# Performance work log

Measured on AMD Instinct MI355X. Metric: run time of the kernel, lower is better.

## Reference

```python
import jax, jax.numpy as jnp
import numpy as np

B, S, D, H = 2048, 200, 64, 4
H1, H2 = 64, 32
F = 4 * D


def _prelu(x, a):
    return jnp.where(x > 0, x, a * x)


def setup_inputs() -> dict:
    key = jax.random.key(0)
    ks = jax.random.split(key, 12)
    inp = {
        "query": jax.random.normal(ks[0], (B, D), dtype=jnp.float32),
        "keys": jax.random.normal(ks[1], (B, S, D), dtype=jnp.float32),
        "keys_mask": jax.random.randint(ks[2], (B, S), 0, 2, dtype=jnp.int32),
        # per-head MLP params (torch Linear equivalent, stored as [in,out])
        "W1": jax.random.normal(ks[3], (H, F, H1), dtype=jnp.float32) / np.sqrt(F),
        "b1": jnp.zeros((H, H1), dtype=jnp.float32),
        "a1": jnp.full((H,), 0.25, dtype=jnp.float32),  # PReLU weight
        "W2": jax.random.normal(ks[4], (H, H1, H2), dtype=jnp.float32) / np.sqrt(H1),
        "b2": jnp.zeros((H, H2), dtype=jnp.float32),
        "a2": jnp.full((H,), 0.25, dtype=jnp.float32),
        "W3": jax.random.normal(ks[5], (H, H2), dtype=jnp.float32) / np.sqrt(H2),
        "b3": jnp.zeros((H,), dtype=jnp.float32),
        # output projection
        "Wo": jax.random.normal(ks[6], (D, D), dtype=jnp.float32) / np.sqrt(D),
        "bo": jnp.zeros((D,), dtype=jnp.float32),
    }
    return inp


def reference(query, keys, keys_mask, W1, b1, a1, W2, b2, a2, W3, b3, Wo, bo):
    # rich attention features: [keys, q, keys*q, keys-q] -> [B,S,4D]
    q = jnp.broadcast_to(query[:, None, :], keys.shape)
    x = jnp.concatenate([keys, q, keys * q, keys - q], axis=-1)
    # all heads at once: tiny per-head MLP with PReLU
    h = jnp.einsum('bsf,hfk->bhsk', x, W1) + b1[None, :, None, :]   # [B,H,S,H1]
    h = _prelu(h, a1[None, :, None, None])
    h = jnp.einsum('bhsk,hkm->bhsm', h, W2) + b2[None, :, None, :]  # [B,H,S,H2]
    h = _prelu(h, a2[None, :, None, None])
    scores = jnp.einsum('bhsm,hm->bhs', h, W3) + b3[None, :, None]  # [B,H,S]
    # mask + softmax + NaN->0 (all-masked rows)
    valid = (keys_mask != 0)[:, None, :]
    scores = jnp.where(valid, scores, -jnp.inf)
    w = jax.nn.softmax(scores, axis=-1)
    w = jnp.where(jnp.isnan(w), jnp.zeros_like(w), w)
    # weighted sum over keys, mean over heads
    out_h = jnp.einsum('bhs,bsd->bhd', w, keys)  # [B,H,D]
    combined = out_h.mean(axis=1)                # [B,D]
    return combined @ Wo + bo
```

## Files before the change

kernel.cpp:

```cpp
#include <hip/hip_runtime.h>
#include <math.h>

constexpr int B  = 2048;
constexpr int S  = 200;
constexpr int D  = 64;
constexpr int H  = 4;
constexpr int H1 = 64;
constexpr int H2 = 32;
constexpr int F  = 256;

constexpr int PK = 72;

typedef short bf16x8 __attribute__((ext_vector_type(8)));
typedef float f32x4  __attribute__((ext_vector_type(4)));
typedef unsigned uint4v __attribute__((ext_vector_type(4)));

__device__ __forceinline__ unsigned cvtpk(float a, float b) {
    unsigned r;
    asm volatile("v_cvt_pk_bf16_f32 %0, %1, %2" : "=v"(r) : "v"(a), "v"(b));
    return r;
}
__device__ __forceinline__ float lo16f(unsigned w) { return __builtin_bit_cast(float, w << 16); }
__device__ __forceinline__ float hi16f(unsigned w) { return __builtin_bit_cast(float, w & 0xffff0000u); }

constexpr size_t SAD_OFF = 0;
constexpr size_t SC_OFF  = SAD_OFF + 4 * 4096 * 4;
constexpr size_t SBD_OFF = SC_OFF  + 4 * 4096 * 4;
constexpr size_t W2I_OFF = SBD_OFF + 4 * 4096 * 4;

__global__ __launch_bounds__(256) void build_kernel(
    const float* __restrict__ W1, const float* __restrict__ W2,
    float* __restrict__ sad, float* __restrict__ sc, float* __restrict__ sbd,
    ushort* __restrict__ w2i)
{
    const int h = blockIdx.x;
    const int t = threadIdx.x;
    const float* w1h = W1 + (size_t)h * F * H1;

    #pragma unroll
    for (int half = 0; half < 2; ++half) {
        const int sl = half * 256 + t;
        const int f  = sl >> 6, l = sl & 63;
        const int mt = f & 3, kk = f >> 2;
        const int k  = 16 * mt + (l & 15);
        const int d0 = 32 * kk + ((l >> 4) << 3);
        float vs[8], vc[8], vb[8];
        #pragma unroll
        for (int j = 0; j < 8; ++j) {
            const int d = d0 + j;
            float A  = w1h[d * 64 + k];
            float Bv = w1h[(64 + d) * 64 + k];
            float C  = w1h[(128 + d) * 64 + k];
            float Dv = w1h[(192 + d) * 64 + k];
            vs[j] = A + Dv; vc[j] = C; vb[j] = Bv - Dv;
        }
        const size_t off = ((size_t)h * 512 + sl) * 8;
        *(f32x4*)&sad[off]     = *(f32x4*)&vs[0];
        *(f32x4*)&sad[off + 4] = *(f32x4*)&vs[4];
        *(f32x4*)&sc [off]     = *(f32x4*)&vc[0];
        *(f32x4*)&sc [off + 4] = *(f32x4*)&vc[4];
        *(f32x4*)&sbd[off]     = *(f32x4*)&vb[0];
        *(f32x4*)&sbd[off + 4] = *(f32x4*)&vb[4];
    }

    {
        const int f2 = t >> 6, l = t & 63;
        const int mt2 = f2 & 1, w = f2 >> 1;
        const int m = 16 * mt2 + (l & 15), k20 = 32 * w + ((l >> 4) << 3);
        const float* w2h = W2 + (size_t)h * H1 * H2;
        uint4v u = { cvtpk(w2h[(k20 + 0) * 32 + m], w2h[(k20 + 1) * 32 + m]),
                     cvtpk(w2h[(k20 + 2) * 32 + m], w2h[(k20 + 3) * 32 + m]),
                     cvtpk(w2h[(k20 + 4) * 32 + m], w2h[(k20 + 5) * 32 + m]),
                     cvtpk(w2h[(k20 + 6) * 32 + m], w2h[(k20 + 7) * 32 + m]) };
        *(uint4v*)&w2i[((size_t)h * 4 + f2) * 512 + l * 8] = u;
    }
}

__global__ __launch_bounds__(256, 3) void fused_b_kernel(
    const float* __restrict__ query, const float* __restrict__ keys,
    const int* __restrict__ mask,
    const float* __restrict__ sad, const float* __restrict__ sc,
    const float* __restrict__ sbd, const ushort* __restrict__ w2i,
    const float* __restrict__ b1, const float* __restrict__ a1,
    const float* __restrict__ b2, const float* __restrict__ a2,
    const float* __restrict__ W3, const float* __restrict__ b3,
    const float* __restrict__ Wo, const float* __restrict__ bo,
    float* __restrict__ out)
{
    __shared__ ushort sK[200 * PK];
    __shared__ ushort relay[4][16 * PK];

    const int b    = blockIdx.x;
    const int t    = threadIdx.x;
    const int lane = t & 63;
    const int h    = t >> 6;
    const int g    = lane >> 4;
    const int ln16 = lane & 15;

    unsigned mbits = 0;
    {
        int mval[4];
        #pragma unroll
        for (int c = 0; c < 4; ++c) {
            int s = lane + 64 * c;
            mval[c] = (s < S) ? mask[(size_t)b * S + s] : 0;
        }
        #pragma unroll
        for (int st = 0; st < 13; ++st) {
            const int src = 16 * (st & 3) + ln16;
            int v = (st >> 2) == 0 ? __shfl(mval[0], src)
                  : (st >> 2) == 1 ? __shfl(mval[1], src)
                  : (st >> 2) == 2 ? __shfl(mval[2], src)
                  :                  __shfl(mval[3], src);
            mbits |= (v != 0) ? (1u << st) : 0u;
        }
    }

    {
        const float4* k4 = (const float4*)(keys + (size_t)b * S * D);
        for (int idx = t; idx < S * D / 4; idx += 256) {
            float4 v = k4[idx];
            int s = idx >> 4, dc = (idx & 15) * 4;
            *(uint2*)&sK[s * PK + dc] = make_uint2(cvtpk(v.x, v.y), cvtpk(v.z, v.w));
        }
    }

    const float* qb = query + (size_t)b * D;
    bf16x8 wh[4][2];
    float qtp0 = 0.f, qtp1 = 0.f, qtp2 = 0.f, qtp3 = 0.f;
    #pragma unroll
    for (int kk = 0; kk < 2; ++kk) {
        const int d0 = 32 * kk + 8 * g;
        f32x4 q0 = *(const f32x4*)&qb[d0];
        f32x4 q1 = *(const f32x4*)&qb[d0 + 4];
        #pragma unroll
        for (int mt = 0; mt < 4; ++mt) {
            const int f = kk * 4 + mt;
            const size_t off = ((size_t)h * 512 + f * 64 + lane) * 8;
            f32x4 s0 = *(const f32x4*)&sad[off], s1 = *(const f32x4*)&sad[off + 4];
            f32x4 c0 = *(const f32x4*)&sc [off], c1 = *(const f32x4*)&sc [off + 4];
            f32x4 bd0 = *(const f32x4*)&sbd[off], bd1 = *(const f32x4*)&sbd[off + 4];
            float w0 = s0[0] + q0[0] * c0[0], w1 = s0[1] + q0[1] * c0[1];
            float w2 = s0[2] + q0[2] * c0[2], w3 = s0[3] + q0[3] * c0[3];
            float w4 = s1[0] + q1[0] * c1[0], w5 = s1[1] + q1[1] * c1[1];
            float w6 = s1[2] + q1[2] * c1[2], w7 = s1[3] + q1[3] * c1[3];
            uint4v u = { cvtpk(w0, w1), cvtpk(w2, w3), cvtpk(w4, w5), cvtpk(w6, w7) };
            wh[mt][kk] = __builtin_bit_cast(bf16x8, u);
            float d = q0[0]*bd0[0] + q0[1]*bd0[1] + q0[2]*bd0[2] + q0[3]*bd0[3]
                    + q1[0]*bd1[0] + q1[1]*bd1[1] + q1[2]*bd1[2] + q1[3]*bd1[3];
            if (mt == 0) qtp0 += d; else if (mt == 1) qtp1 += d;
            else if (mt == 2) qtp2 += d; else qtp3 += d;
        }
    }
    qtp0 += __shfl_xor(qtp0, 16); qtp0 += __shfl_xor(qtp0, 32);
    qtp1 += __shfl_xor(qtp1, 16); qtp1 += __shfl_xor(qtp1, 32);
    qtp2 += __shfl_xor(qtp2, 16); qtp2 += __shfl_xor(qtp2, 32);
    qtp3 += __shfl_xor(qtp3, 16); qtp3 += __shfl_xor(qtp3, 32);
    f32x4 qtv[4];
    #pragma unroll
    for (int mt = 0; mt < 4; ++mt) {
        float src = (mt == 0) ? qtp0 : (mt == 1) ? qtp1 : (mt == 2) ? qtp2 : qtp3;
        f32x4 b1v = *(const f32x4*)&b1[h * 64 + mt * 16 + 4 * g];
        f32x4 v;
        #pragma unroll
        for (int i = 0; i < 4; ++i) v[i] = __shfl(src, 4 * g + i) + b1v[i];
        qtv[mt] = v;
    }

    bf16x8 w2f[2][2];
    #pragma unroll
    for (int w = 0; w < 2; ++w)
        #pragma unroll
        for (int mt2 = 0; mt2 < 2; ++mt2)
            w2f[w][mt2] = *(const bf16x8*)&w2i[((size_t)h * 4 + w * 2 + mt2) * 512 + lane * 8];
    f32x4 b2v[2], w3v[2];
    #pragma unroll
    for (int mt2 = 0; mt2 < 2; ++mt2) {
        b2v[mt2] = *(const f32x4*)&b2[h * 32 + mt2 * 16 + 4 * g];
        w3v[mt2] = *(const f32x4*)&W3[h * 32 + mt2 * 16 + 4 * g];
    }
    const float a1v = a1[h], a2v = a2[h], b3v = b3[h];

    __syncthreads();

    ushort* myR = relay[h];
    float sc13[13];

    #pragma unroll
    for (int st = 0; st < 13; ++st) {
        int srow = st * 16 + ln16;
        srow = srow > 199 ? 199 : srow;
        bf16x8 bk0 = *(const bf16x8*)&sK[srow * PK + 0  + 8 * g];
        bf16x8 bk1 = *(const bf16x8*)&sK[srow * PK + 32 + 8 * g];

        f32x4 acc[4] = { qtv[0], qtv[1], qtv[2], qtv[3] };
        #pragma unroll
        for (int mt = 0; mt < 4; ++mt)
            acc[mt] = __builtin_amdgcn_mfma_f32_16x16x32_bf16(wh[mt][0], bk0, acc[mt], 0, 0, 0);
        #pragma unroll
        for (int mt = 0; mt < 4; ++mt)
            acc[mt] = __builtin_amdgcn_mfma_f32_16x16x32_bf16(wh[mt][1], bk1, acc[mt], 0, 0, 0);

        #pragma unroll
        for (int mt = 0; mt < 4; ++mt) {
            float v0 = acc[mt][0]; v0 = v0 > 0.f ? v0 : a1v * v0;
            float v1 = acc[mt][1]; v1 = v1 > 0.f ? v1 : a1v * v1;
            float v2 = acc[mt][2]; v2 = v2 > 0.f ? v2 : a1v * v2;
            float v3 = acc[mt][3]; v3 = v3 > 0.f ? v3 : a1v * v3;
            *(uint2*)&myR[ln16 * PK + mt * 16 + 4 * g] =
                make_uint2(cvtpk(v0, v1), cvtpk(v2, v3));
        }

        f32x4 acc2[2] = { b2v[0], b2v[1] };
        #pragma unroll
        for (int w = 0; w < 2; ++w) {
            bf16x8 Bh = *(const bf16x8*)&myR[ln16 * PK + w * 32 + 8 * g];
            #pragma unroll
            for (int mt2 = 0; mt2 < 2; ++mt2)
                acc2[mt2] = __builtin_amdgcn_mfma_f32_16x16x32_bf16(w2f[w][mt2], Bh, acc2[mt2], 0, 0, 0);
        }

        float part = 0.f;
        #pragma unroll
        for (int mt2 = 0; mt2 < 2; ++mt2) {
            #pragma unroll
            for (int i = 0; i < 4; ++i) {
                float v = acc2[mt2][i];
                v = v > 0.f ? v : a2v * v;
                part += v * w3v[mt2][i];
            }
        }
        part += __shfl_xor(part, 16);
        part += __shfl_xor(part, 32);
        sc13[st] = part + b3v;
    }

    float* ws = (float*)myR;
    {
        float M = -INFINITY;
        #pragma unroll
        for (int st = 0; st < 13; ++st)
            if ((mbits >> st) & 1) M = fmaxf(M, sc13[st]);
        #pragma unroll
        for (int off = 1; off < 16; off <<= 1) M = fmaxf(M, __shfl_xor(M, off));
        float Z = 0.f;
        #pragma unroll
        for (int st = 0; st < 13; ++st)
            Z += ((mbits >> st) & 1) ? __expf(sc13[st] - M) : 0.f;
        #pragma unroll
        for (int off = 1; off < 16; off <<= 1) Z += __shfl_xor(Z, off);
        const float inv = Z > 0.f ? 1.f / Z : 0.f;
        if (g == 0) {
            #pragma unroll
            for (int st = 0; st < 13; ++st) {
                const int s = st * 16 + ln16;
                if (st < 12 || ln16 < 8)
                    ws[s] = ((mbits >> st) & 1) ? __expf(sc13[st] - M) * inv : 0.f;
            }
        }
    }

    {
        const int sg = lane >> 4, dq = ln16;
        float ax = 0.f, ay = 0.f, az = 0.f, aw = 0.f;
        #pragma unroll 5
        for (int i = 0; i < 50; ++i) {
            const int s = sg * 50 + i;
            const float w = ws[s];
            uint2 kv = *(const uint2*)&sK[s * PK + 4 * dq];
            ax += w * lo16f(kv.x); ay += w * hi16f(kv.x);
            az += w * lo16f(kv.y); aw += w * hi16f(kv.y);
        }
        ax += __shfl_xor(ax, 16); ay += __shfl_xor(ay, 16);
        az += __shfl_xor(az, 16); aw += __shfl_xor(aw, 16);
        ax += __shfl_xor(ax, 32); ay += __shfl_xor(ay, 32);
        az += __shfl_xor(az, 32); aw += __shfl_xor(aw, 32);
        if (lane < 16) {
            float4 o = { ax, ay, az, aw };
            *(float4*)&ws[200 + 4 * dq] = o;
        }
    }
    __syncthreads();

    {
        float p = 0.f;
        #pragma unroll
        for (int j = 0; j < 16; ++j) {
            const int d = 16 * h + j;
            const float cmb = 0.25f * (((const float*)relay[0])[200 + d]
                                     + ((const float*)relay[1])[200 + d]
                                     + ((const float*)relay[2])[200 + d]
                                     + ((const float*)relay[3])[200 + d]);
            p += cmb * Wo[d * 64 + lane];
        }
        ws[264 + lane] = p;
    }
    __syncthreads();
    if (t < 64) {
        float o = bo[t] + ((const float*)relay[0])[264 + t]
                        + ((const float*)relay[1])[264 + t]
                        + ((const float*)relay[2])[264 + t]
                        + ((const float*)relay[3])[264 + t];
        out[(size_t)b * D + t] = o;
    }
}

extern "C" void kernel_launch(void* const* d_in, const int* in_sizes, int n_in,
                              void* d_out, int out_size, void* d_ws, size_t ws_size,
                              hipStream_t stream) {
    const float* query = (const float*)d_in[0];
    const float* keys  = (const float*)d_in[1];
    const int*   mask  = (const int*)d_in[2];
    const float* W1 = (const float*)d_in[3];
    const float* b1 = (const float*)d_in[4];
    const float* a1 = (const float*)d_in[5];
    const float* W2 = (const float*)d_in[6];
    const float* b2 = (const float*)d_in[7];
    const float* a2 = (const float*)d_in[8];
    const float* W3 = (const float*)d_in[9];
    const float* b3 = (const float*)d_in[10];
    const float* Wo = (const float*)d_in[11];
    const float* bo = (const float*)d_in[12];

    float* out  = (float*)d_out;
    char*  ws   = (char*)d_ws;
    float* sad  = (float*)(ws + SAD_OFF);
    float* sc   = (float*)(ws + SC_OFF);
    float* sbd  = (float*)(ws + SBD_OFF);
    ushort* w2i = (ushort*)(ws + W2I_OFF);

    build_kernel<<<dim3(H), 256, 0, stream>>>(W1, W2, sad, sc, sbd, w2i);
    fused_b_kernel<<<dim3(B), 256, 0, stream>>>(
        query, keys, mask, sad, sc, sbd, w2i, b1, a1, b2, a2, W3, b3,
        Wo, bo, out);
}
```

Measured before the change: 64.63 us.

## Split each head across two waves with 512-thread blocks and shared-memory softmax

Doubles the block to 512 threads so each head is handled by two waves, each scoring about half of the 200 keys (7 row tiles each, with one overlapping tile). Scores now go to shared memory, and a separate softmax pass runs on one wave per head with an extra block barrier. The weighted key sum and output projection are split across 8 waves. The key load is unrolled into batched float4 loads, and PReLU uses fmaxf. This aims to raise per-block parallelism and latency hiding, at the cost of extra barriers, duplicated per-wave weight registers, and redundant work on the overlapping tile.

```diff
diff --git a/kernel.cpp b/kernel.cpp
--- a/kernel.cpp
+++ b/kernel.cpp
@@ -76,7 +76,7 @@
     }
 }
 
-__global__ __launch_bounds__(256, 3) void fused_b_kernel(
+__global__ __launch_bounds__(512, 5) void fused_b_kernel(
     const float* __restrict__ query, const float* __restrict__ keys,
     const int* __restrict__ mask,
     const float* __restrict__ sad, const float* __restrict__ sc,
@@ -88,40 +88,47 @@
     float* __restrict__ out)
 {
     __shared__ ushort sK[200 * PK];
-    __shared__ ushort relay[4][16 * PK];
+    __shared__ ushort relay[8][16 * PK];
+    __shared__ float  sSc[4][208];
 
     const int b    = blockIdx.x;
     const int t    = threadIdx.x;
     const int lane = t & 63;
-    const int h    = t >> 6;
+    const int wave = t >> 6;
+    const int h    = wave >> 1;
+    const int sub  = wave & 1;
     const int g    = lane >> 4;
     const int ln16 = lane & 15;
 
-    unsigned mbits = 0;
-    {
-        int mval[4];
+    int mval[4] = {0, 0, 0, 0};
+    if (sub == 0) {
         #pragma unroll
         for (int c = 0; c < 4; ++c) {
             int s = lane + 64 * c;
             mval[c] = (s < S) ? mask[(size_t)b * S + s] : 0;
         }
-        #pragma unroll
-        for (int st = 0; st < 13; ++st) {
-            const int src = 16 * (st & 3) + ln16;
-            int v = (st >> 2) == 0 ? __shfl(mval[0], src)
-                  : (st >> 2) == 1 ? __shfl(mval[1], src)
-                  : (st >> 2) == 2 ? __shfl(mval[2], src)
-                  :                  __shfl(mval[3], src);
-            mbits |= (v != 0) ? (1u << st) : 0u;
-        }
     }
 
     {
         const float4* k4 = (const float4*)(keys + (size_t)b * S * D);
-        for (int idx = t; idx < S * D / 4; idx += 256) {
-            float4 v = k4[idx];
-            int s = idx >> 4, dc = (idx & 15) * 4;
-            *(uint2*)&sK[s * PK + dc] = make_uint2(cvtpk(v.x, v.y), cvtpk(v.z, v.w));
+        float4 kv[6];
+        #pragma unroll
+        for (int i = 0; i < 6; ++i) kv[i] = k4[t + 512 * i];
+        float4 kt;
+        const bool tl = t < 128;
+        if (tl) kt = k4[3072 + t];
+        #pragma unroll
+        for (int i = 0; i < 6; ++i) {
+            const int idx = t + 512 * i;
+            const int s = idx >> 4, dc = (idx & 15) * 4;
+            *(uint2*)&sK[s * PK + dc] =
+                make_uint2(cvtpk(kv[i].x, kv[i].y), cvtpk(kv[i].z, kv[i].w));
+        }
+        if (tl) {
+            const int idx = 3072 + t;
+            const int s = idx >> 4, dc = (idx & 15) * 4;
+            *(uint2*)&sK[s * PK + dc] =
+                make_uint2(cvtpk(kt.x, kt.y), cvtpk(kt.z, kt.w));
         }
     }
 
@@ -183,11 +190,11 @@
 
     __syncthreads();
 
-    ushort* myR = relay[h];
-    float sc13[13];
-
-    #pragma unroll
-    for (int st = 0; st < 13; ++st) {
+    ushort* myR = relay[wave];
+
+    #pragma unroll
+    for (int i = 0; i < 7; ++i) {
+        const int st = 6 * sub + i;
         int srow = st * 16 + ln16;
         srow = srow > 199 ? 199 : srow;
         bf16x8 bk0 = *(const bf16x8*)&sK[srow * PK + 0  + 8 * g];
@@ -203,10 +210,10 @@
 
         #pragma unroll
         for (int mt = 0; mt < 4; ++mt) {
-            float v0 = acc[mt][0]; v0 = v0 > 0.f ? v0 : a1v * v0;
-            float v1 = acc[mt][1]; v1 = v1 > 0.f ? v1 : a1v * v1;
-            float v2 = acc[mt][2]; v2 = v2 > 0.f ? v2 : a1v * v2;
-            float v3 = acc[mt][3]; v3 = v3 > 0.f ? v3 : a1v * v3;
+            float v0 = fmaxf(acc[mt][0], acc[mt][0] * a1v);
+            float v1 = fmaxf(acc[mt][1], acc[mt][1] * a1v);
+            float v2 = fmaxf(acc[mt][2], acc[mt][2] * a1v);
+            float v3 = fmaxf(acc[mt][3], acc[mt][3] * a1v);
             *(uint2*)&myR[ln16 * PK + mt * 16 + 4 * g] =
                 make_uint2(cvtpk(v0, v1), cvtpk(v2, v3));
         }
@@ -224,49 +231,49 @@
         #pragma unroll
         for (int mt2 = 0; mt2 < 2; ++mt2) {
             #pragma unroll
-            for (int i = 0; i < 4; ++i) {
-                float v = acc2[mt2][i];
-                v = v > 0.f ? v : a2v * v;
-                part += v * w3v[mt2][i];
+            for (int i2 = 0; i2 < 4; ++i2) {
+                float v = fmaxf(acc2[mt2][i2], acc2[mt2][i2] * a2v);
+                part += v * w3v[mt2][i2];
             }
         }
         part += __shfl_xor(part, 16);
         part += __shfl_xor(part, 32);
-        sc13[st] = part + b3v;
-    }
-
-    float* ws = (float*)myR;
+        const int s = st * 16 + ln16;
+        if (lane < 16 && s < 200) sSc[h][s] = part + b3v;
+    }
+    __syncthreads();
+
+    if (sub == 0) {
+        float v[4];
+        float M = -INFINITY;
+        #pragma unroll
+        for (int c = 0; c < 4; ++c) {
+            int s = lane + 64 * c;
+            v[c] = (s < S && mval[c]) ? sSc[h][s] : -INFINITY;
+            M = fmaxf(M, v[c]);
+        }
+        #pragma unroll
+        for (int off = 32; off > 0; off >>= 1) M = fmaxf(M, __shfl_xor(M, off));
+        float Z = 0.f, e[4];
+        #pragma unroll
+        for (int c = 0; c < 4; ++c) { e[c] = mval[c] ? __expf(v[c] - M) : 0.f; Z += e[c]; }
+        #pragma unroll
+        for (int off = 32; off > 0; off >>= 1) Z += __shfl_xor(Z, off);
+        const float inv = Z > 0.f ? 1.f / Z : 0.f;
+        #pragma unroll
+        for (int c = 0; c < 4; ++c) { int s = lane + 64 * c; if (s < S) sSc[h][s] = e[c] * inv; }
+    }
+    __syncthreads();
+
+    float* myF = (float*)myR;
     {
-        float M = -INFINITY;
-        #pragma unroll
-        for (int st = 0; st < 13; ++st)
-            if ((mbits >> st) & 1) M = fmaxf(M, sc13[st]);
-        #pragma unroll
-        for (int off = 1; off < 16; off <<= 1) M = fmaxf(M, __shfl_xor(M, off));
-        float Z = 0.f;
-        #pragma unroll
-        for (int st = 0; st < 13; ++st)
-            Z += ((mbits >> st) & 1) ? __expf(sc13[st] - M) : 0.f;
-        #pragma unroll
-        for (int off = 1; off < 16; off <<= 1) Z += __shfl_xor(Z, off);
-        const float inv = Z > 0.f ? 1.f / Z : 0.f;
-        if (g == 0) {
-            #pragma unroll
-            for (int st = 0; st < 13; ++st) {
-                const int s = st * 16 + ln16;
-                if (st < 12 || ln16 < 8)
-                    ws[s] = ((mbits >> st) & 1) ? __expf(sc13[st] - M) * inv : 0.f;
-            }
-        }
-    }
-
-    {
+        const float* wsb = sSc[h];
         const int sg = lane >> 4, dq = ln16;
         float ax = 0.f, ay = 0.f, az = 0.f, aw = 0.f;
         #pragma unroll 5
-        for (int i = 0; i < 50; ++i) {
-            const int s = sg * 50 + i;
-            const float w = ws[s];
+        for (int i = 0; i < 25; ++i) {
+            const int s = 100 * sub + sg * 25 + i;
+            const float w = wsb[s];
             uint2 kv = *(const uint2*)&sK[s * PK + 4 * dq];
             ax += w * lo16f(kv.x); ay += w * hi16f(kv.x);
             az += w * lo16f(kv.y); aw += w * hi16f(kv.y);
@@ -277,7 +284,7 @@
         az += __shfl_xor(az, 32); aw += __shfl_xor(aw, 32);
         if (lane < 16) {
             float4 o = { ax, ay, az, aw };
-            *(float4*)&ws[200 + 4 * dq] = o;
+            *(float4*)&myF[200 + 4 * dq] = o;
         }
     }
     __syncthreads();
@@ -285,22 +292,22 @@
     {
         float p = 0.f;
         #pragma unroll
-        for (int j = 0; j < 16; ++j) {
-            const int d = 16 * h + j;
-            const float cmb = 0.25f * (((const float*)relay[0])[200 + d]
-                                     + ((const float*)relay[1])[200 + d]
-                                     + ((const float*)relay[2])[200 + d]
-                                     + ((const float*)relay[3])[200 + d]);
-            p += cmb * Wo[d * 64 + lane];
-        }
-        ws[264 + lane] = p;
+        for (int j = 0; j < 8; ++j) {
+            const int d = 8 * wave + j;
+            float cmb = 0.f;
+            #pragma unroll
+            for (int w2 = 0; w2 < 8; ++w2)
+                cmb += ((const float*)relay[w2])[200 + d];
+            p += 0.25f * cmb * Wo[d * 64 + lane];
+        }
+        myF[264 + lane] = p;
     }
     __syncthreads();
     if (t < 64) {
-        float o = bo[t] + ((const float*)relay[0])[264 + t]
-                        + ((const float*)relay[1])[264 + t]
-                        + ((const float*)relay[2])[264 + t]
-                        + ((const float*)relay[3])[264 + t];
+        float o = bo[t];
+        #pragma unroll
+        for (int w2 = 0; w2 < 8; ++w2)
+            o += ((const float*)relay[w2])[264 + t];
         out[(size_t)b * D + t] = o;
     }
 }
@@ -330,7 +337,7 @@
     ushort* w2i = (ushort*)(ws + W2I_OFF);
 
     build_kernel<<<dim3(H), 256, 0, stream>>>(W1, W2, sad, sc, sbd, w2i);
-    fused_b_kernel<<<dim3(B), 256, 0, stream>>>(
+    fused_b_kernel<<<dim3(B), 512, 0, stream>>>(
         query, keys, mask, sad, sc, sbd, w2i, b1, a1, b2, a2, W3, b3,
         Wo, bo, out);
 }
```

New measurement: 214.4 us. 232% more time.
